# Performance work log

Hardware: AMD Instinct MI355X
Metric: run time of the kernel (lower is better)

The kernel has to match this reference:

```python
import jax, jax.numpy as jnp
import numpy as np

B, T, C = 2, 2048, 2048
H, G = 32, 8
D = C // H  # 64


def _rope_freqs(t, d_half, theta=10000.0):
    inv = 1.0 / (theta ** (np.arange(0, d_half, dtype=np.float32) / d_half * 2.0 / 2.0 * 2.0))
    # standard: freqs_i = theta^(-2i/D) for i in [0, D/2)
    inv = 1.0 / (theta ** (2.0 * np.arange(d_half, dtype=np.float32) / (2 * d_half)))
    ang = np.outer(np.arange(t, dtype=np.float32), inv)  # [T, D/2]
    return jnp.asarray(np.cos(ang)), jnp.asarray(np.sin(ang))


def setup_inputs() -> dict:
    key = jax.random.key(0)
    ks = jax.random.split(key, 5)
    s = 0.02
    cos, sin = _rope_freqs(T, D // 2)
    return {
        "x": jax.random.normal(ks[0], (B, T, C), jnp.float32),
        "freqs_cos": cos,
        "freqs_sin": sin,
        "mask": jnp.ones((1, 1), jnp.bool_),  # non-None mask -> causal attention
        "Wq": jax.random.normal(ks[1], (C, C), jnp.float32) * s,
        "Wk": jax.random.normal(ks[2], (C, G * D), jnp.float32) * s,
        "Wv": jax.random.normal(ks[3], (C, G * D), jnp.float32) * s,
        "Wo": jax.random.normal(ks[4], (C, C), jnp.float32) * s,
    }


def _apply_rope(x, cos, sin):
    # x: [B, T, N, D]; pairs (x[..., 2i], x[..., 2i+1]) rotated by angle[t, i]
    b, t, n, d = x.shape
    xr = x.astype(jnp.float32).reshape(b, t, n, d // 2, 2)
    x0, x1 = xr[..., 0], xr[..., 1]
    c = cos[:t][None, :, None, :]
    s = sin[:t][None, :, None, :]
    out = jnp.stack([x0 * c - x1 * s, x0 * s + x1 * c], axis=-1)
    return out.reshape(b, t, n, d).astype(x.dtype)


def reference(x, freqs_cos, freqs_sin, mask, Wq, Wk, Wv, Wo):
    b, t, c = x.shape
    q = (x @ Wq).reshape(b, t, H, D)
    k = (x @ Wk).reshape(b, t, G, D)
    v = (x @ Wv).reshape(b, t, G, D)
    q = _apply_rope(q, freqs_cos, freqs_sin)
    k = _apply_rope(k, freqs_cos, freqs_sin)
    k_cache, v_cache = k, v  # new_kv_cache (pre-expansion)
    # GQA expansion: repeat_interleave along head dim
    rep = H // G
    ke = jnp.repeat(k, rep, axis=2)  # [B, T, H, D]
    ve = jnp.repeat(v, rep, axis=2)
    scale = 1.0 / jnp.sqrt(jnp.asarray(D, x.dtype))
    scores = jnp.einsum("bqhd,bkhd->bhqk", q, ke) * scale  # [B, H, T, T]
    causal = jnp.tril(jnp.ones((t, t), jnp.bool_))
    scores = jnp.where(causal[None, None], scores, jnp.finfo(scores.dtype).min)
    attn = jax.nn.softmax(scores, axis=-1)
    out = jnp.einsum("bhqk,bkhd->bqhd", attn, ve).reshape(b, t, c)
    return out @ Wo, k_cache, v_cache
```

## Files before the change

### kernel.cpp

```cpp
#include <hip/hip_runtime.h>
#include <cstdint>
#include <cstddef>

typedef unsigned short ushort_t;
typedef signed char s8;
typedef __attribute__((ext_vector_type(4))) float f32x4;
typedef __attribute__((ext_vector_type(16))) float f32x16;
typedef __attribute__((ext_vector_type(8))) short short8;
typedef __attribute__((ext_vector_type(4))) float float4_t;
typedef __attribute__((ext_vector_type(4))) unsigned short ushort4_t;
typedef __attribute__((ext_vector_type(2))) unsigned int uint2v;
typedef __attribute__((ext_vector_type(4))) int int4v;
typedef __attribute__((ext_vector_type(2))) int int2v;

#define KD 2048
#define TT 2048
#define NH 32
#define NG 8

__device__ __forceinline__ ushort_t f2bf(float f) {
  union { float f; uint32_t u; } cv; cv.f = f;
  uint32_t u = cv.u;
  return (ushort_t)((u + 0x7FFFu + ((u >> 16) & 1u)) >> 16);
}

__device__ __forceinline__ float bf2f(ushort_t v) {
  union { uint32_t u; float f; } cv; cv.u = ((uint32_t)v) << 16;
  return cv.f;
}

__device__ __forceinline__ uint32_t cvtpk(float a, float b) {
  uint32_t r;
  asm("v_cvt_pk_bf16_f32 %0, %1, %2" : "=v"(r) : "v"(a), "v"(b));
  return r;
}

__device__ __forceinline__ float exp2fast(float x) {
  float r;
  asm("v_exp_f32 %0, %1" : "=v"(r) : "v"(x));
  return r;
}

__device__ __forceinline__ float max3f(float a, float b, float c) {
  return fmaxf(fmaxf(a, b), c);
}

__device__ __forceinline__ void gload_lds16(const void* g, void* l) {
  __builtin_amdgcn_global_load_lds(
      (const __attribute__((address_space(1))) unsigned int*)g,
      (__attribute__((address_space(3))) unsigned int*)l, 16, 0, 0);
}

__global__ __launch_bounds__(256) void xq_kernel(const float* __restrict__ x,
                                                 s8* __restrict__ xq,
                                                 float* __restrict__ xs) {
  const int row = blockIdx.x;
  const int tid = threadIdx.x;
  const float* src = x + (size_t)row * 2048 + tid * 8;
  float4_t a = *(const float4_t*)(src);
  float4_t b = *(const float4_t*)(src + 4);
  float m = fmaxf(fmaxf(fmaxf(fabsf(a[0]), fabsf(a[1])), fmaxf(fabsf(a[2]), fabsf(a[3]))),
                  fmaxf(fmaxf(fabsf(b[0]), fabsf(b[1])), fmaxf(fabsf(b[2]), fabsf(b[3]))));
#pragma unroll
  for (int st = 32; st > 0; st >>= 1) m = fmaxf(m, __shfl_xor(m, st));
  __shared__ float red[4];
  if ((tid & 63) == 0) red[tid >> 6] = m;
  __syncthreads();
  m = fmaxf(fmaxf(red[0], red[1]), fmaxf(red[2], red[3]));
  const float inv = (m > 0.f) ? 127.f / m : 0.f;
  union { s8 c[8]; int2v v; } pk;
#pragma unroll
  for (int i = 0; i < 4; ++i) {
    pk.c[i]     = (s8)__float2int_rn(a[i] * inv);
    pk.c[4 + i] = (s8)__float2int_rn(b[i] * inv);
  }
  *(int2v*)(xq + (size_t)row * 2048 + tid * 8) = pk.v;
  if (tid == 0) xs[row] = (m > 0.f) ? m / 127.f : 0.f;
}

__global__ __launch_bounds__(256) void wq_kernel(const ushort_t* __restrict__ wt,
                                                 s8* __restrict__ wq,
                                                 float* __restrict__ wqs) {
  const int row = blockIdx.x;
  const int tid = threadIdx.x;
  short8 v8 = *(const short8*)(wt + (size_t)row * 2048 + tid * 8);
  float f[8];
#pragma unroll
  for (int i = 0; i < 8; ++i) f[i] = bf2f((ushort_t)v8[i]);
  float m = 0.f;
#pragma unroll
  for (int i = 0; i < 8; ++i) m = fmaxf(m, fabsf(f[i]));
#pragma unroll
  for (int st = 32; st > 0; st >>= 1) m = fmaxf(m, __shfl_xor(m, st));
  __shared__ float red[4];
  if ((tid & 63) == 0) red[tid >> 6] = m;
  __syncthreads();
  m = fmaxf(fmaxf(red[0], red[1]), fmaxf(red[2], red[3]));
  const float inv = (m > 0.f) ? 127.f / m : 0.f;
  union { s8 c[8]; int2v v; } pk;
#pragma unroll
  for (int i = 0; i < 8; ++i) pk.c[i] = (s8)__float2int_rn(f[i] * inv);
  *(int2v*)(wq + (size_t)row * 2048 + tid * 8) = pk.v;
  if (tid == 0) wqs[row] = (m > 0.f) ? m / 127.f : 0.f;
}

__global__ __launch_bounds__(256) void cvt_wt_kernel(const float* __restrict__ Wq,
                                                     const float* __restrict__ Wk,
                                                     const float* __restrict__ Wv,
                                                     const float* __restrict__ Wo,
                                                     ushort_t* __restrict__ wqkvT,
                                                     ushort_t* __restrict__ woT) {
  __shared__ float tile[32][33];
  const int bid = blockIdx.x;
  const float* src;
  ushort_t* dst;
  int Nc, bx, by;
  if (bid < 4096)      { src = Wq; dst = wqkvT;                       Nc = 2048; int r = bid;        bx = r & 63; by = r >> 6; }
  else if (bid < 5120) { src = Wk; dst = wqkvT + (size_t)2048 * KD;   Nc = 512;  int r = bid - 4096; bx = r & 15; by = r >> 4; }
  else if (bid < 6144) { src = Wv; dst = wqkvT + (size_t)2560 * KD;   Nc = 512;  int r = bid - 5120; bx = r & 15; by = r >> 4; }
  else                 { src = Wo; dst = woT;                         Nc = 2048; int r = bid - 6144; bx = r & 63; by = r >> 6; }
  const int tx = threadIdx.x, ty = threadIdx.y;
  const int c0 = bx * 32, r0 = by * 32;
#pragma unroll
  for (int i = 0; i < 4; i++)
    tile[ty + i * 8][tx] = src[(size_t)(r0 + ty + i * 8) * Nc + c0 + tx];
  __syncthreads();
#pragma unroll
  for (int i = 0; i < 4; i++)
    dst[(size_t)(c0 + ty + i * 8) * KD + r0 + tx] = f2bf(tile[tx][ty + i * 8]);
}

__global__ __launch_bounds__(256) void vtrans_kernel(const ushort_t* __restrict__ v,
                                                     ushort_t* __restrict__ vt) {
  __shared__ ushort_t tile[64][72];
  const int bg = blockIdx.y;
  const int t0 = blockIdx.x * 64;
  const ushort_t* src = v + ((size_t)bg * TT + t0) * 64;
#pragma unroll
  for (int i = 0; i < 2; ++i) {
    int p = i * 256 + threadIdx.x;
    int r = p >> 3, c = (p & 7) * 8;
    *(short8*)&tile[r][c] = *(const short8*)(src + r * 64 + c);
  }
  __syncthreads();
  ushort_t* dst = vt + (size_t)bg * 64 * TT + t0;
#pragma unroll
  for (int i = 0; i < 2; ++i) {
    int p = i * 256 + threadIdx.x;
    int d = p >> 3, c = (p & 7) * 8;
    short8 o;
#pragma unroll
    for (int j = 0; j < 8; ++j) o[j] = tile[c + j][d];
    *(short8*)(dst + (size_t)d * TT + c) = o;
  }
}

template <int MODE, int BN>
__global__ __launch_bounds__(512, 4) void gemmq_kernel(
    const s8* __restrict__ A, const s8* __restrict__ Bt,
    const float* __restrict__ sa, const float* __restrict__ sb,
    const float* __restrict__ cosT, const float* __restrict__ sinT,
    ushort_t* __restrict__ q_ws, ushort_t* __restrict__ k_ws,
    ushort_t* __restrict__ v_ws, float* __restrict__ kcache,
    float* __restrict__ vcache, float* __restrict__ outF) {
  constexpr int NT = 16;
  constexpr int CW = BN / 4;
  constexpr int MF = 4;
  constexpr int NF = CW / 16;
  constexpr int AGL = 2;
  constexpr int BGL = BN / 64;
  constexpr int GL = AGL + BGL;
  constexpr int ASZ = 128 * 128;
  constexpr int BSZ = BN * 128;
  __shared__ s8 sA[2 * ASZ];
  __shared__ s8 sB[2 * BSZ];
  const int tid = threadIdx.x;
  const int lane = tid & 63;
  const int w = tid >> 6;
  const int wm = w >> 2, wn = w & 3;
  const int bid = blockIdx.x;
  const int j = bid >> 3;
  const int by = 4 * (bid & 7) + (j & 3);
  const int bx = j >> 2;
  const int rowBase = by * 128;
  const int colBase = bx * BN;

  int aRO[AGL], aLO[AGL];
#pragma unroll
  for (int i = 0; i < AGL; ++i) {
    int c = i * 512 + tid;
    int r = c >> 3, lc = (c & 7) ^ (r & 7);
    aRO[i] = r * 2048 + lc * 16;
    aLO[i] = (i * 512 + (tid & ~63)) * 16;
  }
  int bRO[BGL], bLO[BGL];
#pragma unroll
  for (int i = 0; i < BGL; ++i) {
    int c = i * 512 + tid;
    int r = c >> 3, lc = (c & 7) ^ (r & 7);
    bRO[i] = r * 2048 + lc * 16;
    bLO[i] = (i * 512 + (tid & ~63)) * 16;
  }

  auto stage = [&](int bb, int kt) {
    const s8* ab = A + (size_t)rowBase * 2048 + kt * 128;
#pragma unroll
    for (int i = 0; i < AGL; ++i)
      gload_lds16(ab + aRO[i], &sA[bb * ASZ + aLO[i]]);
    const s8* bbp = Bt + (size_t)colBase * 2048 + kt * 128;
#pragma unroll
    for (int i = 0; i < BGL; ++i)
      gload_lds16(bbp + bRO[i], &sB[bb * BSZ + bLO[i]]);
  };

  int4v acc[MF][NF];
#pragma unroll
  for (int i = 0; i < MF; i++)
#pragma unroll
    for (int j2 = 0; j2 < NF; j2++) acc[i][j2] = int4v{0, 0, 0, 0};

  stage(0, 0);

  for (int k = 0; k < NT; ++k) {
    const int buf = k & 1;
    if (k + 1 < NT) {
      stage(buf ^ 1, k + 1);
      asm volatile("s_waitcnt vmcnt(%0)" :: "n"(GL) : "memory");
    } else {
      asm volatile("s_waitcnt vmcnt(0)" ::: "memory");
    }
    __builtin_amdgcn_s_barrier();

    const s8* Abuf = &sA[buf * ASZ];
    const s8* Bbuf = &sB[buf * BSZ];
#pragma unroll
    for (int ks = 0; ks < 2; ++ks) {
      int4v bfr[NF], af[MF];
#pragma unroll
      for (int ni = 0; ni < NF; ++ni) {
        int n = wn * CW + ni * 16 + (lane & 15);
        bfr[ni] = *(const int4v*)(&Bbuf[n * 128 +
            (((ks * 4 + (lane >> 4)) ^ (n & 7)) * 16)]);
      }
#pragma unroll
      for (int mi = 0; mi < MF; ++mi) {
        int r = wm * 64 + mi * 16 + (lane & 15);
        af[mi] = *(const int4v*)(&Abuf[r * 128 +
            (((ks * 4 + (lane >> 4)) ^ (r & 7)) * 16)]);
      }
      __builtin_amdgcn_s_setprio(1);
#pragma unroll
      for (int mi = 0; mi < MF; ++mi)
#pragma unroll
        for (int ni = 0; ni < NF; ++ni)
          acc[mi][ni] = __builtin_amdgcn_mfma_i32_16x16x64_i8(
              af[mi], bfr[ni], acc[mi][ni], 0, 0, 0);
      __builtin_amdgcn_s_setprio(0);
    }
    __builtin_amdgcn_s_barrier();
  }

#pragma unroll
  for (int mi = 0; mi < MF; ++mi) {
    int rg0 = rowBase + wm * 64 + mi * 16 + ((lane >> 4) * 4);
    float sar[4];
#pragma unroll
    for (int jj = 0; jj < 4; ++jj) sar[jj] = sa[rg0 + jj];
#pragma unroll
    for (int ni = 0; ni < NF; ++ni) {
      int cg = colBase + wn * CW + ni * 16 + (lane & 15);
      const float sbc = sb[cg];
      int4v v4 = acc[mi][ni];
#pragma unroll
      for (int j2 = 0; j2 < 4; ++j2) {
        float v = (float)v4[j2] * sar[j2] * sbc;
        int row = rg0 + j2;
        if constexpr (MODE == 0) {
          float pv = __shfl_xor(v, 1);
          int bb2 = row >> 11, tq = row & (TT - 1);
          int d = cg & 63, i2 = d >> 1;
          if (cg < 2048) {
            float cc = cosT[tq * 32 + i2], ss = sinT[tq * 32 + i2];
            float out = (d & 1) ? (pv * ss + v * cc) : (v * cc - pv * ss);
            int hh = cg >> 6;
            q_ws[(((size_t)(bb2 * NH + hh)) * TT + tq) * 64 + d] = f2bf(out * 0.18033688f);
          } else if (cg < 2560) {
            float cc = cosT[tq * 32 + i2], ss = sinT[tq * 32 + i2];
            float out = (d & 1) ? (pv * ss + v * cc) : (v * cc - pv * ss);
            int gg = (cg - 2048) >> 6;
            kcache[(((size_t)(bb2 * TT + tq)) * NG + gg) * 64 + d] = out;
            k_ws[(((size_t)(bb2 * NG + gg)) * TT + tq) * 64 + d] = f2bf(out);
          } else {
            int gg = (cg - 2560) >> 6;
            vcache[(((size_t)(bb2 * TT + tq)) * NG + gg) * 64 + d] = v;
            v_ws[(((size_t)(bb2 * NG + gg)) * TT + tq) * 64 + d] = f2bf(v);
          }
        } else {
          outF[(size_t)row * 2048 + cg] = v;
        }
      }
    }
  }
}

#define PACK(SV, E, OUT)                                        \
  {                                                             \
    uint32_t A0 = cvtpk(SV[8 * E + 0], SV[8 * E + 1]);          \
    uint32_t A1 = cvtpk(SV[8 * E + 2], SV[8 * E + 3]);          \
    uint32_t B0 = cvtpk(SV[8 * E + 4], SV[8 * E + 5]);          \
    uint32_t B1 = cvtpk(SV[8 * E + 6], SV[8 * E + 7]);          \
    asm("v_permlane32_swap_b32 %0, %1" : "+v"(A0), "+v"(B0));   \
    asm("v_permlane32_swap_b32 %0, %1" : "+v"(A1), "+v"(B1));   \
    union { uint32_t u[4]; short8 s8v; } UU;                    \
    UU.u[0] = A0; UU.u[1] = A1; UU.u[2] = B0; UU.u[3] = B1;     \
    OUT = UU.s8v;                                               \
  }

__global__ __launch_bounds__(256, 4) void attn_kernel(const ushort_t* __restrict__ qw,
                                                      const ushort_t* __restrict__ kw,
                                                      const ushort_t* __restrict__ vtw,
                                                      ushort_t* __restrict__ attn) {
  __shared__ ushort_t sK[2][4096];
  __shared__ ushort_t sVT[2][4096];
  const int tid = threadIdx.x;
  const int lane = tid & 63;
  const int w = tid >> 6;
  const int hi = lane >> 5;
  const int col = lane & 31;
  const int bid = blockIdx.x;
  const int xcd = bid & 7;
  const int b3 = (bid >> 3) & 1;
  const int rep = (bid >> 4) & 3;
  const int w2 = (bid >> 6) & 3;
  const int u = (bid >> 8) & 3;
  const int qt = (u & 1) ? (2 * w2 + (u >> 1)) : (15 - 2 * w2 - (u >> 1));
  const int pair = 2 * xcd + b3;
  const int b = pair >> 3, g = pair & 7;
  const int h = g * 4 + rep;
  const int q0w = qt * 128 + w * 32;
  const int qg = q0w + col;
  const int ntiles = 2 * qt + 2;

  const ushort_t* qbase = qw + ((size_t)(b * NH + h) * TT + qg) * 64;
  const ushort_t* kbase = kw + (size_t)(b * NG + g) * TT * 64;
  const ushort_t* vtbase = vtw + (size_t)(b * NG + g) * 64 * TT;

  short8 qf[4];
#pragma unroll
  for (int dsub = 0; dsub < 4; ++dsub)
    qf[dsub] = *(const short8*)(qbase + dsub * 16 + hi * 8);

  const int r0 = tid >> 3;
  const int cl = (tid & 7) ^ (r0 & 7);
  const ushort_t* kS0 = kbase + r0 * 64 + cl * 8;
  const ushort_t* kS1 = kbase + (r0 + 32) * 64 + cl * 8;
  const ushort_t* vS0 = vtbase + (size_t)r0 * TT + cl * 8;
  const ushort_t* vS1 = vtbase + (size_t)(r0 + 32) * TT + cl * 8;
  const int off0 = (tid & ~63) * 8;
  const int off1 = off0 + 2048;

  auto stage = [&](int bb, int k0) {
    gload_lds16(kS0 + (size_t)k0 * 64, &sK[bb][off0]);
    gload_lds16(kS1 + (size_t)k0 * 64, &sK[bb][off1]);
    gload_lds16(vS0 + k0, &sVT[bb][off0]);
    gload_lds16(vS1 + k0, &sVT[bb][off1]);
  };

  f32x16 o0 = {};
  f32x16 o1 = {};
  f32x16 l16 = {};
  float m_run = -3.0e38f;

  stage(0, 0);
  asm volatile("s_waitcnt vmcnt(0)" ::: "memory");
  __syncthreads();

  for (int kt = 0; kt < ntiles; ++kt) {
    const int k0 = kt * 64;
    const int buf = kt & 1;
    if (kt + 1 < ntiles) stage(buf ^ 1, k0 + 64);
    if (k0 <= q0w + 31) {
      const ushort_t* K = sK[buf];
      const ushort_t* V = sVT[buf];
      f32x16 s0 = {};
      f32x16 s1 = {};
      __builtin_amdgcn_s_setprio(1);
#pragma unroll
      for (int dsub = 0; dsub < 4; ++dsub) {
        const int ch = dsub * 2 + hi;
        const int sw = ((ch ^ (col & 7)) * 8);
        short8 a0 = *(const short8*)(K + col * 64 + sw);
        short8 a1 = *(const short8*)(K + (32 + col) * 64 + sw);
        s0 = __builtin_amdgcn_mfma_f32_32x32x16_bf16(a0, qf[dsub], s0, 0, 0, 0);
        s1 = __builtin_amdgcn_mfma_f32_32x32x16_bf16(a1, qf[dsub], s1, 0, 0, 0);
      }
      __builtin_amdgcn_s_setprio(0);
      if (k0 + 63 > q0w) {
#pragma unroll
        for (int r = 0; r < 16; ++r) {
          int key5 = (r & 3) + 8 * (r >> 2) + 4 * hi;
          if (k0 + key5 > qg) s0[r] = -3.0e38f;
          if (k0 + 32 + key5 > qg) s1[r] = -3.0e38f;
        }
      }
      float p0 = max3f(s0[0], s0[1], s0[2]);
      float p1 = max3f(s0[3], s0[4], s0[5]);
      float p2 = max3f(s0[6], s0[7], s0[8]);
      float p3 = max3f(s0[9], s0[10], s0[11]);
      float p4 = max3f(s0[12], s0[13], s0[14]);
      float p5 = max3f(s1[0], s1[1], s1[2]);
      float p6 = max3f(s1[3], s1[4], s1[5]);
      float p7 = max3f(s1[6], s1[7], s1[8]);
      float p8 = max3f(s1[9], s1[10], s1[11]);
      float p9 = max3f(s1[12], s1[13], s1[14]);
      float pa = fmaxf(s0[15], s1[15]);
      float q0 = max3f(p0, p1, p2);
      float q1 = max3f(p3, p4, p5);
      float q2 = max3f(p6, p7, p8);
      float q3 = max3f(p9, pa, q0);
      float mtl = max3f(q1, q2, q3);
      float mt = fmaxf(mtl, __shfl_xor(mtl, 32));
      if (!__all(mt - m_run <= 8.0f)) {
        float mn = fmaxf(m_run, mt);
        float al = exp2fast(m_run - mn);
        m_run = mn;
#pragma unroll
        for (int r = 0; r < 16; ++r) { o0[r] *= al; o1[r] *= al; l16[r] *= al; }
      }
#pragma unroll
      for (int r = 0; r < 16; ++r) {
        s0[r] = exp2fast(s0[r] - m_run);
        s1[r] = exp2fast(s1[r] - m_run);
        l16[r] += s0[r] + s1[r];
      }
      short8 pb;
      const int swz = (col & 7);
#define PVMM(KS)                                                            \
  {                                                                         \
    const int ch = KS * 2 + hi;                                             \
    const int so = ((ch ^ swz) * 8);                                        \
    short8 va = *(const short8*)(V + col * 64 + so);                        \
    short8 vb = *(const short8*)(V + (32 + col) * 64 + so);                 \
    __builtin_amdgcn_s_setprio(1);                                          \
    o0 = __builtin_amdgcn_mfma_f32_32x32x16_bf16(va, pb, o0, 0, 0, 0);      \
    o1 = __builtin_amdgcn_mfma_f32_32x32x16_bf16(vb, pb, o1, 0, 0, 0);      \
    __builtin_amdgcn_s_setprio(0);                                          \
  }
      PACK(s0, 0, pb); PVMM(0)
      PACK(s0, 1, pb); PVMM(1)
      PACK(s1, 0, pb); PVMM(2)
      PACK(s1, 1, pb); PVMM(3)
#undef PVMM
    }
    asm volatile("s_waitcnt vmcnt(0)" ::: "memory");
    __syncthreads();
  }

  float l4[4];
#pragma unroll
  for (int r = 0; r < 4; ++r)
    l4[r] = (l16[4 * r] + l16[4 * r + 1]) + (l16[4 * r + 2] + l16[4 * r + 3]);
  float lsum = (l4[0] + l4[1]) + (l4[2] + l4[3]);
  float l_run = lsum + __shfl_xor(lsum, 32);
  const float inv = 1.f / l_run;
  ushort_t* obase = attn + ((size_t)b * TT + qg) * 2048 + h * 64;
#pragma unroll
  for (int g4 = 0; g4 < 4; ++g4) {
    int d = g4 * 8 + hi * 4;
    uint2v u2v;
    u2v[0] = cvtpk(o0[4 * g4 + 0] * inv, o0[4 * g4 + 1] * inv);
    u2v[1] = cvtpk(o0[4 * g4 + 2] * inv, o0[4 * g4 + 3] * inv);
    *(uint2v*)(obase + d) = u2v;
    uint2v u2b;
    u2b[0] = cvtpk(o1[4 * g4 + 0] * inv, o1[4 * g4 + 1] * inv);
    u2b[1] = cvtpk(o1[4 * g4 + 2] * inv, o1[4 * g4 + 3] * inv);
    *(uint2v*)(obase + 32 + d) = u2b;
  }
}

extern "C" void kernel_launch(void* const* d_in, const int* in_sizes, int n_in,
                              void* d_out, int out_size, void* d_ws, size_t ws_size,
                              hipStream_t stream) {
  (void)in_sizes; (void)n_in; (void)out_size; (void)ws_size;
  const float* x    = (const float*)d_in[0];
  const float* cosT = (const float*)d_in[1];
  const float* sinT = (const float*)d_in[2];
  const float* Wq   = (const float*)d_in[4];
  const float* Wk   = (const float*)d_in[5];
  const float* Wv   = (const float*)d_in[6];
  const float* Wo   = (const float*)d_in[7];

  float* outF   = (float*)d_out;
  float* kcache = outF + (size_t)8388608;
  float* vcache = kcache + (size_t)2097152;

  uint8_t* ws = (uint8_t*)d_ws;
  s8*       xq     = (s8*)(ws);
  float*    xs     = (float*)(ws + 8388608);
  float*    wqs    = (float*)(ws + 8388608 + 65536);
  float*    wos    = (float*)(ws + 8388608 + 131072);
  float*    as_s   = (float*)(ws + 8388608 + 196608);
  ushort_t* vt_ws  = (ushort_t*)(ws + 9437184);
  ushort_t* wqkvT  = (ushort_t*)(ws + 16777216);
  ushort_t* attn_ws= (ushort_t*)(ws + 16777216);
  s8*       wq_q   = (s8*)(ws + 35651584);
  ushort_t* q_ws   = (ushort_t*)(ws + 41943040);
  s8*       aq     = (s8*)(ws + 41943040);
  ushort_t* k_ws   = (ushort_t*)(ws + 58720256);
  ushort_t* v_ws   = (ushort_t*)(ws + 62914560);
  ushort_t* woT    = (ushort_t*)(ws + 67108864);
  s8*       wo_q   = (s8*)(ws + 75497472);

  xq_kernel<<<4096, 256, 0, stream>>>(x, xq, xs);
  cvt_wt_kernel<<<10240, dim3(32, 8), 0, stream>>>(Wq, Wk, Wv, Wo, wqkvT, woT);
  wq_kernel<<<3072, 256, 0, stream>>>(wqkvT, wq_q, wqs);
  wq_kernel<<<2048, 256, 0, stream>>>(woT, wo_q, wos);

  gemmq_kernel<0, 192><<<512, 512, 0, stream>>>(xq, wq_q, xs, wqs, cosT, sinT,
                                                q_ws, k_ws, v_ws, kcache, vcache,
                                                nullptr);
  vtrans_kernel<<<dim3(32, 16), 256, 0, stream>>>(v_ws, vt_ws);
  attn_kernel<<<1024, 256, 0, stream>>>(q_ws, k_ws, vt_ws, attn_ws);
  wq_kernel<<<4096, 256, 0, stream>>>(attn_ws, aq, as_s);
  gemmq_kernel<1, 128><<<512, 512, 0, stream>>>(aq, wo_q, as_s, wos, nullptr, nullptr,
                                                nullptr, nullptr, nullptr, nullptr,
                                                nullptr, outF);
}
```

Measured before the change: 159.1 us.

## Merge prep kernels and widen attention key tiles to 128

Fuses the x-quantize and weight transpose/convert kernels into one launch, and the two weight-quantize launches into another, cutting four launches down to two. The attention kernel now processes 128-key tiles with doubled LDS buffers and four score accumulators. Each block handles one 128-query tile in simple descending order instead of the previous interleaved pairing. This halves loop iterations and barriers and applies the causal mask only on the last tile. In exchange, LDS use doubles, occupancy drops (launch bounds 4 to 2) and register pressure rises, and the last tile may waste more masked work.

```diff
diff --git a/kernel.cpp b/kernel.cpp
--- a/kernel.cpp
+++ b/kernel.cpp
@@ -51,16 +51,81 @@
       (__attribute__((address_space(3))) unsigned int*)l, 16, 0, 0);
 }
 
-__global__ __launch_bounds__(256) void xq_kernel(const float* __restrict__ x,
-                                                 s8* __restrict__ xq,
-                                                 float* __restrict__ xs) {
-  const int row = blockIdx.x;
+__global__ __launch_bounds__(256) void prep1_kernel(const float* __restrict__ x,
+                                                    s8* __restrict__ xq,
+                                                    float* __restrict__ xs,
+                                                    const float* __restrict__ Wq,
+                                                    const float* __restrict__ Wk,
+                                                    const float* __restrict__ Wv,
+                                                    const float* __restrict__ Wo,
+                                                    ushort_t* __restrict__ wqkvT,
+                                                    ushort_t* __restrict__ woT) {
   const int tid = threadIdx.x;
-  const float* src = x + (size_t)row * 2048 + tid * 8;
-  float4_t a = *(const float4_t*)(src);
-  float4_t b = *(const float4_t*)(src + 4);
-  float m = fmaxf(fmaxf(fmaxf(fabsf(a[0]), fabsf(a[1])), fmaxf(fabsf(a[2]), fabsf(a[3]))),
-                  fmaxf(fmaxf(fabsf(b[0]), fabsf(b[1])), fmaxf(fabsf(b[2]), fabsf(b[3]))));
+  if (blockIdx.x < 4096) {
+    const int row = blockIdx.x;
+    const float* src = x + (size_t)row * 2048 + tid * 8;
+    float4_t a = *(const float4_t*)(src);
+    float4_t b = *(const float4_t*)(src + 4);
+    float m = fmaxf(fmaxf(fmaxf(fabsf(a[0]), fabsf(a[1])), fmaxf(fabsf(a[2]), fabsf(a[3]))),
+                    fmaxf(fmaxf(fabsf(b[0]), fabsf(b[1])), fmaxf(fabsf(b[2]), fabsf(b[3]))));
+#pragma unroll
+    for (int st = 32; st > 0; st >>= 1) m = fmaxf(m, __shfl_xor(m, st));
+    __shared__ float red[4];
+    if ((tid & 63) == 0) red[tid >> 6] = m;
+    __syncthreads();
+    m = fmaxf(fmaxf(red[0], red[1]), fmaxf(red[2], red[3]));
+    const float inv = (m > 0.f) ? 127.f / m : 0.f;
+    union { s8 c[8]; int2v v; } pk;
+#pragma unroll
+    for (int i = 0; i < 4; ++i) {
+      pk.c[i]     = (s8)__float2int_rn(a[i] * inv);
+      pk.c[4 + i] = (s8)__float2int_rn(b[i] * inv);
+    }
+    *(int2v*)(xq + (size_t)row * 2048 + tid * 8) = pk.v;
+    if (tid == 0) xs[row] = (m > 0.f) ? m / 127.f : 0.f;
+    return;
+  }
+  __shared__ float tile[32][33];
+  const int bid = blockIdx.x - 4096;
+  const float* src;
+  ushort_t* dst;
+  int Nc, bx, by;
+  if (bid < 4096)      { src = Wq; dst = wqkvT;                       Nc = 2048; int r = bid;        bx = r & 63; by = r >> 6; }
+  else if (bid < 5120) { src = Wk; dst = wqkvT + (size_t)2048 * KD;   Nc = 512;  int r = bid - 4096; bx = r & 15; by = r >> 4; }
+  else if (bid < 6144) { src = Wv; dst = wqkvT + (size_t)2560 * KD;   Nc = 512;  int r = bid - 5120; bx = r & 15; by = r >> 4; }
+  else                 { src = Wo; dst = woT;                         Nc = 2048; int r = bid - 6144; bx = r & 63; by = r >> 6; }
+  const int tx = tid & 31, ty = tid >> 5;
+  const int c0 = bx * 32, r0 = by * 32;
+#pragma unroll
+  for (int i = 0; i < 4; i++)
+    tile[ty + i * 8][tx] = src[(size_t)(r0 + ty + i * 8) * Nc + c0 + tx];
+  __syncthreads();
+#pragma unroll
+  for (int i = 0; i < 4; i++)
+    dst[(size_t)(c0 + ty + i * 8) * KD + r0 + tx] = f2bf(tile[tx][ty + i * 8]);
+}
+
+__global__ __launch_bounds__(256) void wqall_kernel(const ushort_t* __restrict__ wqkvT,
+                                                    const ushort_t* __restrict__ woT,
+                                                    s8* __restrict__ wq_q,
+                                                    s8* __restrict__ wo_q,
+                                                    float* __restrict__ wqs,
+                                                    float* __restrict__ wos) {
+  const int bid = blockIdx.x;
+  const ushort_t* wt;
+  s8* wq;
+  float* sc;
+  int row;
+  if (bid < 3072) { wt = wqkvT; wq = wq_q; sc = wqs; row = bid; }
+  else            { wt = woT;   wq = wo_q; sc = wos; row = bid - 3072; }
+  const int tid = threadIdx.x;
+  short8 v8 = *(const short8*)(wt + (size_t)row * 2048 + tid * 8);
+  float f[8];
+#pragma unroll
+  for (int i = 0; i < 8; ++i) f[i] = bf2f((ushort_t)v8[i]);
+  float m = 0.f;
+#pragma unroll
+  for (int i = 0; i < 8; ++i) m = fmaxf(m, fabsf(f[i]));
 #pragma unroll
   for (int st = 32; st > 0; st >>= 1) m = fmaxf(m, __shfl_xor(m, st));
   __shared__ float red[4];
@@ -70,12 +135,9 @@
   const float inv = (m > 0.f) ? 127.f / m : 0.f;
   union { s8 c[8]; int2v v; } pk;
 #pragma unroll
-  for (int i = 0; i < 4; ++i) {
-    pk.c[i]     = (s8)__float2int_rn(a[i] * inv);
-    pk.c[4 + i] = (s8)__float2int_rn(b[i] * inv);
-  }
-  *(int2v*)(xq + (size_t)row * 2048 + tid * 8) = pk.v;
-  if (tid == 0) xs[row] = (m > 0.f) ? m / 127.f : 0.f;
+  for (int i = 0; i < 8; ++i) pk.c[i] = (s8)__float2int_rn(f[i] * inv);
+  *(int2v*)(wq + (size_t)row * 2048 + tid * 8) = pk.v;
+  if (tid == 0) sc[row] = (m > 0.f) ? m / 127.f : 0.f;
 }
 
 __global__ __launch_bounds__(256) void wq_kernel(const ushort_t* __restrict__ wt,
@@ -102,32 +164,6 @@
   for (int i = 0; i < 8; ++i) pk.c[i] = (s8)__float2int_rn(f[i] * inv);
   *(int2v*)(wq + (size_t)row * 2048 + tid * 8) = pk.v;
   if (tid == 0) wqs[row] = (m > 0.f) ? m / 127.f : 0.f;
-}
-
-__global__ __launch_bounds__(256) void cvt_wt_kernel(const float* __restrict__ Wq,
-                                                     const float* __restrict__ Wk,
-                                                     const float* __restrict__ Wv,
-                                                     const float* __restrict__ Wo,
-                                                     ushort_t* __restrict__ wqkvT,
-                                                     ushort_t* __restrict__ woT) {
-  __shared__ float tile[32][33];
-  const int bid = blockIdx.x;
-  const float* src;
-  ushort_t* dst;
-  int Nc, bx, by;
-  if (bid < 4096)      { src = Wq; dst = wqkvT;                       Nc = 2048; int r = bid;        bx = r & 63; by = r >> 6; }
-  else if (bid < 5120) { src = Wk; dst = wqkvT + (size_t)2048 * KD;   Nc = 512;  int r = bid - 4096; bx = r & 15; by = r >> 4; }
-  else if (bid < 6144) { src = Wv; dst = wqkvT + (size_t)2560 * KD;   Nc = 512;  int r = bid - 5120; bx = r & 15; by = r >> 4; }
-  else                 { src = Wo; dst = woT;                         Nc = 2048; int r = bid - 6144; bx = r & 63; by = r >> 6; }
-  const int tx = threadIdx.x, ty = threadIdx.y;
-  const int c0 = bx * 32, r0 = by * 32;
-#pragma unroll
-  for (int i = 0; i < 4; i++)
-    tile[ty + i * 8][tx] = src[(size_t)(r0 + ty + i * 8) * Nc + c0 + tx];
-  __syncthreads();
-#pragma unroll
-  for (int i = 0; i < 4; i++)
-    dst[(size_t)(c0 + ty + i * 8) * KD + r0 + tx] = f2bf(tile[tx][ty + i * 8]);
 }
 
 __global__ __launch_bounds__(256) void vtrans_kernel(const ushort_t* __restrict__ v,
@@ -316,30 +352,26 @@
     OUT = UU.s8v;                                               \
   }
 
-__global__ __launch_bounds__(256, 4) void attn_kernel(const ushort_t* __restrict__ qw,
+__global__ __launch_bounds__(256, 2) void attn_kernel(const ushort_t* __restrict__ qw,
                                                       const ushort_t* __restrict__ kw,
                                                       const ushort_t* __restrict__ vtw,
                                                       ushort_t* __restrict__ attn) {
-  __shared__ ushort_t sK[2][4096];
-  __shared__ ushort_t sVT[2][4096];
+  __shared__ ushort_t sK[2][8192];
+  __shared__ ushort_t sVT[2][8192];
   const int tid = threadIdx.x;
   const int lane = tid & 63;
   const int w = tid >> 6;
   const int hi = lane >> 5;
   const int col = lane & 31;
   const int bid = blockIdx.x;
-  const int xcd = bid & 7;
-  const int b3 = (bid >> 3) & 1;
+  const int pair = 2 * (bid & 7) + ((bid >> 3) & 1);
   const int rep = (bid >> 4) & 3;
-  const int w2 = (bid >> 6) & 3;
-  const int u = (bid >> 8) & 3;
-  const int qt = (u & 1) ? (2 * w2 + (u >> 1)) : (15 - 2 * w2 - (u >> 1));
-  const int pair = 2 * xcd + b3;
+  const int qt = 15 - (bid >> 6);
   const int b = pair >> 3, g = pair & 7;
   const int h = g * 4 + rep;
   const int q0w = qt * 128 + w * 32;
   const int qg = q0w + col;
-  const int ntiles = 2 * qt + 2;
+  const int ntiles = qt + 1;
 
   const ushort_t* qbase = qw + ((size_t)(b * NH + h) * TT + qg) * 64;
   const ushort_t* kbase = kw + (size_t)(b * NG + g) * TT * 64;
@@ -350,20 +382,24 @@
   for (int dsub = 0; dsub < 4; ++dsub)
     qf[dsub] = *(const short8*)(qbase + dsub * 16 + hi * 8);
 
-  const int r0 = tid >> 3;
-  const int cl = (tid & 7) ^ (r0 & 7);
-  const ushort_t* kS0 = kbase + r0 * 64 + cl * 8;
-  const ushort_t* kS1 = kbase + (r0 + 32) * 64 + cl * 8;
-  const ushort_t* vS0 = vtbase + (size_t)r0 * TT + cl * 8;
-  const ushort_t* vS1 = vtbase + (size_t)(r0 + 32) * TT + cl * 8;
-  const int off0 = (tid & ~63) * 8;
-  const int off1 = off0 + 2048;
+  int kRO[4], vRO[4], sOF[4];
+#pragma unroll
+  for (int i = 0; i < 4; ++i) {
+    int c = i * 256 + tid;
+    int kr = c >> 3, kc = (c & 7) ^ (kr & 7);
+    kRO[i] = kr * 64 + kc * 8;
+    int vr = c >> 4, vc = (c & 15) ^ (vr & 15);
+    vRO[i] = vr * 2048 + vc * 8;
+    sOF[i] = (i * 256 + (tid & ~63)) * 8;
+  }
 
   auto stage = [&](int bb, int k0) {
-    gload_lds16(kS0 + (size_t)k0 * 64, &sK[bb][off0]);
-    gload_lds16(kS1 + (size_t)k0 * 64, &sK[bb][off1]);
-    gload_lds16(vS0 + k0, &sVT[bb][off0]);
-    gload_lds16(vS1 + k0, &sVT[bb][off1]);
+#pragma unroll
+    for (int i = 0; i < 4; ++i)
+      gload_lds16(kbase + (size_t)k0 * 64 + kRO[i], &sK[bb][sOF[i]]);
+#pragma unroll
+    for (int i = 0; i < 4; ++i)
+      gload_lds16(vtbase + k0 + vRO[i], &sVT[bb][sOF[i]]);
   };
 
   f32x16 o0 = {};
@@ -376,82 +412,84 @@
   __syncthreads();
 
   for (int kt = 0; kt < ntiles; ++kt) {
-    const int k0 = kt * 64;
+    const int k0 = kt * 128;
     const int buf = kt & 1;
-    if (kt + 1 < ntiles) stage(buf ^ 1, k0 + 64);
-    if (k0 <= q0w + 31) {
-      const ushort_t* K = sK[buf];
-      const ushort_t* V = sVT[buf];
-      f32x16 s0 = {};
-      f32x16 s1 = {};
-      __builtin_amdgcn_s_setprio(1);
-#pragma unroll
-      for (int dsub = 0; dsub < 4; ++dsub) {
-        const int ch = dsub * 2 + hi;
-        const int sw = ((ch ^ (col & 7)) * 8);
-        short8 a0 = *(const short8*)(K + col * 64 + sw);
-        short8 a1 = *(const short8*)(K + (32 + col) * 64 + sw);
-        s0 = __builtin_amdgcn_mfma_f32_32x32x16_bf16(a0, qf[dsub], s0, 0, 0, 0);
-        s1 = __builtin_amdgcn_mfma_f32_32x32x16_bf16(a1, qf[dsub], s1, 0, 0, 0);
+    if (kt + 1 < ntiles) stage(buf ^ 1, k0 + 128);
+    const ushort_t* K = sK[buf];
+    const ushort_t* V = sVT[buf];
+    f32x16 s0 = {}, s1 = {}, s2 = {}, s3 = {};
+    __builtin_amdgcn_s_setprio(1);
+#pragma unroll
+    for (int dsub = 0; dsub < 4; ++dsub) {
+      const int ch = dsub * 2 + hi;
+#pragma unroll
+      for (int kb = 0; kb < 4; ++kb) {
+        int kr = kb * 32 + col;
+        short8 a = *(const short8*)(K + kr * 64 + ((ch ^ (kr & 7)) * 8));
+        if (kb == 0) s0 = __builtin_amdgcn_mfma_f32_32x32x16_bf16(a, qf[dsub], s0, 0, 0, 0);
+        if (kb == 1) s1 = __builtin_amdgcn_mfma_f32_32x32x16_bf16(a, qf[dsub], s1, 0, 0, 0);
+        if (kb == 2) s2 = __builtin_amdgcn_mfma_f32_32x32x16_bf16(a, qf[dsub], s2, 0, 0, 0);
+        if (kb == 3) s3 = __builtin_amdgcn_mfma_f32_32x32x16_bf16(a, qf[dsub], s3, 0, 0, 0);
       }
-      __builtin_amdgcn_s_setprio(0);
-      if (k0 + 63 > q0w) {
-#pragma unroll
-        for (int r = 0; r < 16; ++r) {
-          int key5 = (r & 3) + 8 * (r >> 2) + 4 * hi;
-          if (k0 + key5 > qg) s0[r] = -3.0e38f;
-          if (k0 + 32 + key5 > qg) s1[r] = -3.0e38f;
-        }
+    }
+    __builtin_amdgcn_s_setprio(0);
+    if (kt == ntiles - 1) {
+#pragma unroll
+      for (int r = 0; r < 16; ++r) {
+        int key5 = (r & 3) + 8 * (r >> 2) + 4 * hi;
+        if (k0 + key5 > qg) s0[r] = -3.0e38f;
+        if (k0 + 32 + key5 > qg) s1[r] = -3.0e38f;
+        if (k0 + 64 + key5 > qg) s2[r] = -3.0e38f;
+        if (k0 + 96 + key5 > qg) s3[r] = -3.0e38f;
       }
-      float p0 = max3f(s0[0], s0[1], s0[2]);
-      float p1 = max3f(s0[3], s0[4], s0[5]);
-      float p2 = max3f(s0[6], s0[7], s0[8]);
-      float p3 = max3f(s0[9], s0[10], s0[11]);
-      float p4 = max3f(s0[12], s0[13], s0[14]);
-      float p5 = max3f(s1[0], s1[1], s1[2]);
-      float p6 = max3f(s1[3], s1[4], s1[5]);
-      float p7 = max3f(s1[6], s1[7], s1[8]);
-      float p8 = max3f(s1[9], s1[10], s1[11]);
-      float p9 = max3f(s1[12], s1[13], s1[14]);
-      float pa = fmaxf(s0[15], s1[15]);
-      float q0 = max3f(p0, p1, p2);
-      float q1 = max3f(p3, p4, p5);
-      float q2 = max3f(p6, p7, p8);
-      float q3 = max3f(p9, pa, q0);
-      float mtl = max3f(q1, q2, q3);
-      float mt = fmaxf(mtl, __shfl_xor(mtl, 32));
-      if (!__all(mt - m_run <= 8.0f)) {
-        float mn = fmaxf(m_run, mt);
-        float al = exp2fast(m_run - mn);
-        m_run = mn;
-#pragma unroll
-        for (int r = 0; r < 16; ++r) { o0[r] *= al; o1[r] *= al; l16[r] *= al; }
-      }
-#pragma unroll
-      for (int r = 0; r < 16; ++r) {
-        s0[r] = exp2fast(s0[r] - m_run);
-        s1[r] = exp2fast(s1[r] - m_run);
-        l16[r] += s0[r] + s1[r];
-      }
-      short8 pb;
-      const int swz = (col & 7);
+    }
+    float tm[16];
+#pragma unroll
+    for (int r = 0; r < 16; ++r)
+      tm[r] = max3f(fmaxf(s0[r], s1[r]), s2[r], s3[r]);
+    float p0 = max3f(tm[0], tm[1], tm[2]);
+    float p1 = max3f(tm[3], tm[4], tm[5]);
+    float p2 = max3f(tm[6], tm[7], tm[8]);
+    float p3 = max3f(tm[9], tm[10], tm[11]);
+    float p4 = max3f(tm[12], tm[13], tm[14]);
+    float mtl = max3f(max3f(p0, p1, p2), max3f(p3, p4, tm[15]), -3.0e38f);
+    float mt = fmaxf(mtl, __shfl_xor(mtl, 32));
+    if (!__all(mt - m_run <= 8.0f)) {
+      float mn = fmaxf(m_run, mt);
+      float al = exp2fast(m_run - mn);
+      m_run = mn;
+#pragma unroll
+      for (int r = 0; r < 16; ++r) { o0[r] *= al; o1[r] *= al; l16[r] *= al; }
+    }
+#pragma unroll
+    for (int r = 0; r < 16; ++r) {
+      s0[r] = exp2fast(s0[r] - m_run);
+      s1[r] = exp2fast(s1[r] - m_run);
+      s2[r] = exp2fast(s2[r] - m_run);
+      s3[r] = exp2fast(s3[r] - m_run);
+      l16[r] += (s0[r] + s1[r]) + (s2[r] + s3[r]);
+    }
+    short8 pb;
 #define PVMM(KS)                                                            \
   {                                                                         \
     const int ch = KS * 2 + hi;                                             \
-    const int so = ((ch ^ swz) * 8);                                        \
-    short8 va = *(const short8*)(V + col * 64 + so);                        \
-    short8 vb = *(const short8*)(V + (32 + col) * 64 + so);                 \
+    short8 va = *(const short8*)(V + col * 128 + ((ch ^ (col & 15)) * 8));  \
+    short8 vb = *(const short8*)(V + (32 + col) * 128 +                     \
+                                 ((ch ^ ((32 + col) & 15)) * 8));           \
     __builtin_amdgcn_s_setprio(1);                                          \
     o0 = __builtin_amdgcn_mfma_f32_32x32x16_bf16(va, pb, o0, 0, 0, 0);      \
     o1 = __builtin_amdgcn_mfma_f32_32x32x16_bf16(vb, pb, o1, 0, 0, 0);      \
     __builtin_amdgcn_s_setprio(0);                                          \
   }
-      PACK(s0, 0, pb); PVMM(0)
-      PACK(s0, 1, pb); PVMM(1)
-      PACK(s1, 0, pb); PVMM(2)
-      PACK(s1, 1, pb); PVMM(3)
+    PACK(s0, 0, pb); PVMM(0)
+    PACK(s0, 1, pb); PVMM(1)
+    PACK(s1, 0, pb); PVMM(2)
+    PACK(s1, 1, pb); PVMM(3)
+    PACK(s2, 0, pb); PVMM(4)
+    PACK(s2, 1, pb); PVMM(5)
+    PACK(s3, 0, pb); PVMM(6)
+    PACK(s3, 1, pb); PVMM(7)
 #undef PVMM
-    }
     asm volatile("s_waitcnt vmcnt(0)" ::: "memory");
     __syncthreads();
   }
@@ -511,10 +549,8 @@
   ushort_t* woT    = (ushort_t*)(ws + 67108864);
   s8*       wo_q   = (s8*)(ws + 75497472);
 
-  xq_kernel<<<4096, 256, 0, stream>>>(x, xq, xs);
-  cvt_wt_kernel<<<10240, dim3(32, 8), 0, stream>>>(Wq, Wk, Wv, Wo, wqkvT, woT);
-  wq_kernel<<<3072, 256, 0, stream>>>(wqkvT, wq_q, wqs);
-  wq_kernel<<<2048, 256, 0, stream>>>(woT, wo_q, wos);
+  prep1_kernel<<<14336, 256, 0, stream>>>(x, xq, xs, Wq, Wk, Wv, Wo, wqkvT, woT);
+  wqall_kernel<<<5120, 256, 0, stream>>>(wqkvT, woT, wq_q, wo_q, wqs, wos);
 
   gemmq_kernel<0, 192><<<512, 512, 0, stream>>>(xq, wq_q, xs, wqs, cosT, sinT,
                                                 q_ws, k_ws, v_ws, kcache, vcache,
```

Result: no change. 159.4 us (+0.2%).
